# Kernel tuning notes

Measured on AMD Instinct MI355X. Metric: run time of the kernel, lower is better.

## Reference

```python
import jax, jax.numpy as jnp
import numpy as np

NB, NA, NC, NH, NW = 32, 5, 80, 76, 76
MAX_OBJ = 50
STRIDE = 32.0
ANCHORS_PX = np.array([18.3274, 21.6763, 59.9827, 66.0010, 106.8298,
                       175.1789, 252.2502, 112.8890, 312.6566, 293.3850], dtype=np.float32)
ANCHORS = (ANCHORS_PX / STRIDE).reshape(NA, 2)  # grid units, as in forward()
NOOBJ_SCALE, OBJ_SCALE = 1.0, 5.0
SIL_THRESH = 0.6
SEEN = 20000
COORD_SCALE, CLASS_SCALE = 1.0, 1.0
WARM = SEEN < 12800  # static python branch, matches `if seen < 12800`


def setup_inputs() -> dict:
    key = jax.random.key(0)
    k1, k2, k3, k4 = jax.random.split(key, 4)
    output = jax.random.normal(k1, (NB, NA * (5 + NC), NH, NW), dtype=jnp.float32) * 0.5
    # target layout per object: [class, cx, cy, w, h], coords normalized to (0,1)
    cls_id = jax.random.randint(k2, (NB, MAX_OBJ, 1), 0, NC).astype(jnp.float32)
    cxy = jax.random.uniform(k3, (NB, MAX_OBJ, 2), minval=0.05, maxval=0.95)
    wh = jax.random.uniform(k4, (NB, MAX_OBJ, 2), minval=0.02, maxval=0.4)
    target = jnp.concatenate([cls_id, cxy, wh], axis=-1).reshape(NB, MAX_OBJ * 5)
    return {"output": output, "target": target}


def _iou_cwh(a, b):
    # boxes as (cx, cy, w, h), broadcastable [..., 4]; darknet bbox_iou(x1y1x2y2=False)
    iw = jnp.maximum(jnp.minimum(a[..., 0] + a[..., 2] * 0.5, b[..., 0] + b[..., 2] * 0.5)
                     - jnp.maximum(a[..., 0] - a[..., 2] * 0.5, b[..., 0] - b[..., 2] * 0.5), 0.0)
    ih = jnp.maximum(jnp.minimum(a[..., 1] + a[..., 3] * 0.5, b[..., 1] + b[..., 3] * 0.5)
                     - jnp.maximum(a[..., 1] - a[..., 3] * 0.5, b[..., 1] - b[..., 3] * 0.5), 0.0)
    inter = iw * ih
    union = a[..., 2] * a[..., 3] + b[..., 2] * b[..., 3] - inter
    return inter / union


def reference(output, target):
    # ---- Part 1: parse raw predictions ----
    out = output.reshape(NB, NA, 5 + NC, NH, NW)
    x = jax.nn.sigmoid(out[:, :, 0])        # [B,A,H,W]
    y = jax.nn.sigmoid(out[:, :, 1])
    w = out[:, :, 2]
    h = out[:, :, 3]
    conf = jax.nn.sigmoid(out[:, :, 4])
    # cls layout matches view(nB*nA,nC,nH*nW).transpose(1,2) -> [B*A*H*W, C]
    cls_logits = jnp.transpose(out[:, :, 5:], (0, 1, 3, 4, 2)).reshape(-1, NC)

    # ---- Part 2: decode boxes (detached, like pred_boxes built from .data) ----
    anchors = jnp.asarray(ANCHORS)
    pbx = x + jnp.arange(NW, dtype=jnp.float32)[None, None, None, :]
    pby = y + jnp.arange(NH, dtype=jnp.float32)[None, None, :, None]
    pbw = jnp.exp(w) * anchors[None, :, 0, None, None]
    pbh = jnp.exp(h) * anchors[None, :, 1, None, None]
    pred_boxes = jax.lax.stop_gradient(jnp.stack([pbx, pby, pbw, pbh], axis=-1))  # [B,A,H,W,4]

    # ---- Part 3: build_targets, fully vectorized ----
    tgt = target.reshape(NB, MAX_OBJ, 5)
    valid = jnp.cumprod(tgt[:, :, 1] > 0, axis=1).astype(bool)  # break at first x==0
    gcls = tgt[:, :, 0]
    gx = tgt[:, :, 1] * NW
    gy = tgt[:, :, 2] * NH
    gw = tgt[:, :, 3] * NW
    gh = tgt[:, :, 4] * NH
    gt = jnp.stack([gx, gy, gw, gh], axis=-1)  # [B,T,4]

    # silence mask: max IoU of every pred box vs every gt box  -> [B,T,A,H,W]
    ious = _iou_cwh(pred_boxes[:, None], gt[:, :, None, None, None, :])
    max_iou = jnp.max(jnp.where(valid[:, :, None, None, None], ious, 0.0), axis=1)
    conf_mask = jnp.where(max_iou > SIL_THRESH, 0.0, NOOBJ_SCALE)  # [B,A,H,W]

    # best anchor per gt: IoU of centered (0,0,w,h) boxes -> closed form
    aw, ah = anchors[:, 0], anchors[:, 1]
    inter = jnp.minimum(gw[..., None], aw) * jnp.minimum(gh[..., None], ah)
    union = gw[..., None] * gh[..., None] + aw * ah - inter
    best_n = jnp.argmax(inter / union, axis=-1)  # [B,T]

    gi = gx.astype(jnp.int32)
    gj = gy.astype(jnp.int32)
    b_idx = jnp.arange(NB)[:, None]
    best_aw = anchors[best_n, 0]
    best_ah = anchors[best_n, 1]
    pred_at = pred_boxes[b_idx, best_n, gj, gi]  # [B,T,4]
    best_iou = _iou_cwh(gt, pred_at)             # [B,T]

    total = NB * NA * NH * NW
    flat = ((b_idx * NA + best_n) * NH + gj) * NW + gi
    flat = jnp.where(valid, flat, total).ravel()  # invalid objects -> dropped

    def scat(base, vals):
        return (jnp.full((total,), base, dtype=jnp.float32)
                .at[flat].set(vals.ravel(), mode='drop')
                .reshape(NB, NA, NH, NW))

    ones_t = jnp.ones_like(gx)
    warm = 1.0 if WARM else 0.0
    coord_mask = scat(warm, ones_t)
    cls_mask = scat(0.0, ones_t)
    tx = scat(0.5 * warm, gx - gi)
    ty = scat(0.5 * warm, gy - gj)
    tw = scat(0.0, jnp.log(gw / best_aw))
    th = scat(0.0, jnp.log(gh / best_ah))
    tconf = scat(0.0, best_iou)
    tcls = scat(0.0, gcls)
    conf_mask = (conf_mask.ravel()
                 .at[flat].set(jnp.full(flat.shape, OBJ_SCALE, dtype=jnp.float32), mode='drop')
                 .reshape(NB, NA, NH, NW))
    conf_mask = jnp.sqrt(conf_mask)

    # ---- Part 4: losses ----
    loss_x = COORD_SCALE * jnp.sum((x * coord_mask - tx * coord_mask) ** 2) / 2.0
    loss_y = COORD_SCALE * jnp.sum((y * coord_mask - ty * coord_mask) ** 2) / 2.0
    loss_w = COORD_SCALE * jnp.sum((w * coord_mask - tw * coord_mask) ** 2) / 2.0
    loss_h = COORD_SCALE * jnp.sum((h * coord_mask - th * coord_mask) ** 2) / 2.0
    loss_conf = jnp.sum((conf * conf_mask - tconf * conf_mask) ** 2) / 2.0
    logp = jax.nn.log_softmax(cls_logits, axis=-1)
    labels = tcls.ravel().astype(jnp.int32)
    nll = -jnp.take_along_axis(logp, labels[:, None], axis=1)[:, 0]
    loss_cls = CLASS_SCALE * jnp.sum(nll * cls_mask.ravel())

    return loss_x + loss_y + loss_w + loss_h + loss_conf + loss_cls
```

## Files before the change

### kernel.cpp

```cpp
#include <hip/hip_runtime.h>
#include <math.h>

#define NBATCH 32
#define NANCH  5
#define NCLS   80
#define NHH    76
#define NWW    76
#define MAXOBJ 50
#define CSZ    (NHH*NWW)
#define CELLS_PER_B (NANCH*CSZ)
#define NCH    (5+NCLS)
#define SILT   0.6f
#define CPT    4
#define BLK    256

__constant__ float c_aw[NANCH] = {18.3274f/32.0f, 59.9827f/32.0f, 106.8298f/32.0f, 252.2502f/32.0f, 312.6566f/32.0f};
__constant__ float c_ah[NANCH] = {21.6763f/32.0f, 66.0010f/32.0f, 175.1789f/32.0f, 112.8890f/32.0f, 293.3850f/32.0f};

__device__ __forceinline__ float sigf(float x) { return 1.0f / (1.0f + __expf(-x)); }

__global__ void obj_kernel(const float* __restrict__ out,
                           const float* __restrict__ tgt,
                           float* __restrict__ loss) {
    __shared__ float T[MAXOBJ*5];
    __shared__ int   key[MAXOBJ];
    const int b = blockIdx.x;
    const int t = threadIdx.x;
    for (int i = t; i < MAXOBJ*5; i += 64) T[i] = tgt[(size_t)b*MAXOBJ*5 + i];
    __syncthreads();

    float gx=0.f, gy=0.f, gw=0.f, gh=0.f;
    int gi=0, gj=0, bn=0, cls=0;
    bool valid = false;
    if (t < MAXOBJ) {
        valid = true;
        for (int j = 0; j <= t; ++j) valid = valid && (T[j*5+1] > 0.0f);
        cls = (int)T[t*5+0];
        gx = T[t*5+1]*NWW; gy = T[t*5+2]*NHH;
        gw = T[t*5+3]*NWW; gh = T[t*5+4]*NHH;
        gi = (int)gx; gj = (int)gy;
        float best = -1.0f;
        for (int a = 0; a < NANCH; ++a) {
            float inter = fminf(gw, c_aw[a]) * fminf(gh, c_ah[a]);
            float uni   = gw*gh + c_aw[a]*c_ah[a] - inter;
            float iou   = inter / uni;
            if (iou > best) { best = iou; bn = a; }
        }
        key[t] = valid ? (bn*CSZ + gj*NWW + gi) : (-1 - t);
    }
    __syncthreads();

    if (t < MAXOBJ && valid) {
        bool owner = true;
        for (int o2 = t+1; o2 < MAXOBJ; ++o2)
            if (key[o2] == key[t]) { owner = false; break; }
        if (owner) {
            const size_t base = ((size_t)(b*NANCH + bn))*NCH*CSZ + (size_t)(gj*NWW + gi);
            float xr = out[base];
            float yr = out[base + (size_t)CSZ];
            float wr = out[base + (size_t)2*CSZ];
            float hr = out[base + (size_t)3*CSZ];
            float cr = out[base + (size_t)4*CSZ];
            float sx = sigf(xr), sy = sigf(yr), sc = sigf(cr);
            float pw = __expf(wr)*c_aw[bn], ph = __expf(hr)*c_ah[bn];
            float px = sx + (float)gi, py = sy + (float)gj;
            float iw = fmaxf(fminf(px+pw*0.5f, gx+gw*0.5f) - fmaxf(px-pw*0.5f, gx-gw*0.5f), 0.0f);
            float ih = fmaxf(fminf(py+ph*0.5f, gy+gh*0.5f) - fmaxf(py-ph*0.5f, gy-gh*0.5f), 0.0f);
            float inter = iw*ih;
            float biou  = inter / (pw*ph + gw*gh - inter);
            float tx = gx - (float)gi, ty = gy - (float)gj;
            float tw = __logf(gw / c_aw[bn]), th = __logf(gh / c_ah[bn]);
            float l = 0.5f*((sx-tx)*(sx-tx) + (sy-ty)*(sy-ty)
                          + (wr-tw)*(wr-tw) + (hr-th)*(hr-th));
            l += 2.5f*(sc - biou)*(sc - biou);
            const float* lg = out + base + (size_t)5*CSZ;
            float m = -1e30f, s = 0.0f, lc = 0.0f;
            for (int c = 0; c < NCLS; ++c) {
                float L = lg[(size_t)c*CSZ];
                if (c == cls) lc = L;
                if (L > m) { s = s*__expf(m - L) + 1.0f; m = L; }
                else       { s += __expf(L - m); }
            }
            l += m + __logf(s) - lc;
            atomicAdd(loss, l);
        }
    }
}

__global__ __launch_bounds__(BLK)
void cell_kernel(const float* __restrict__ out,
                 const float* __restrict__ tgt,
                 float* __restrict__ loss) {
    __shared__ float  T[MAXOBJ*5];
    __shared__ float4 sbox[MAXOBJ];
    __shared__ float2 sak[MAXOBJ];
    __shared__ float  wsum[BLK/64];
    const int b = blockIdx.y;
    const int t = threadIdx.x;
    for (int i = t; i < MAXOBJ*5; i += BLK) T[i] = tgt[(size_t)b*MAXOBJ*5 + i];
    __syncthreads();
    if (t < MAXOBJ) {
        bool valid = true;
        for (int j = 0; j <= t; ++j) valid = valid && (T[j*5+1] > 0.0f);
        float gx = T[t*5+1]*NWW, gy = T[t*5+2]*NHH;
        float gw = T[t*5+3]*NWW, gh = T[t*5+4]*NHH;
        int bn = 0; float best = -1.0f;
        for (int a = 0; a < NANCH; ++a) {
            float inter = fminf(gw, c_aw[a]) * fminf(gh, c_ah[a]);
            float uni   = gw*gh + c_aw[a]*c_ah[a] - inter;
            float iou   = inter / uni;
            if (iou > best) { best = iou; bn = a; }
        }
        int k = valid ? (bn*CSZ + ((int)gy)*NWW + (int)gx) : (-1 - t);
        if (valid) {
            sbox[t] = make_float4(gx - gw*0.5f, gy - gh*0.5f, gx + gw*0.5f, gy + gh*0.5f);
            sak[t]  = make_float2(gw*gh, __int_as_float(k));
        } else {
            sbox[t] = make_float4(3e8f, 3e8f, 3e8f, 3e8f);
            sak[t]  = make_float2(1.0f, __int_as_float(k));
        }
    }
    __syncthreads();

    const int c0 = blockIdx.x*(BLK*CPT) + t;
    float px1[CPT], py1[CPT], px2[CPT], py2[CPT], pa[CPT], crs[CPT];
    int cc[CPT]; bool live[CPT];
    #pragma unroll
    for (int k = 0; k < CPT; ++k) {
        const int c = c0 + k*BLK;
        cc[k] = c;
        live[k] = (c < CELLS_PER_B);
        float xr=0.f, yr=0.f, wr=0.f, hr=0.f, cr=0.f;
        int a = 0;
        if (live[k]) {
            a = c / CSZ;
            const int rem = c - a*CSZ;
            const size_t base = ((size_t)(b*NANCH + a))*NCH*CSZ + (size_t)rem;
            xr = out[base];
            yr = out[base + (size_t)CSZ];
            wr = out[base + (size_t)2*CSZ];
            hr = out[base + (size_t)3*CSZ];
            cr = out[base + (size_t)4*CSZ];
        }
        const int rem = c - a*CSZ;
        const int i = rem % NWW;
        const int j = rem / NWW;
        float pw = __expf(wr)*c_aw[a], ph = __expf(hr)*c_ah[a];
        float px = sigf(xr) + (float)i, py = sigf(yr) + (float)j;
        px1[k] = px - pw*0.5f; px2[k] = px + pw*0.5f;
        py1[k] = py - ph*0.5f; py2[k] = py + ph*0.5f;
        pa[k]  = pw*ph; crs[k] = cr;
    }

    bool sil[CPT], own[CPT];
    #pragma unroll
    for (int k = 0; k < CPT; ++k) { sil[k] = false; own[k] = false; }

    for (int o = 0; o < MAXOBJ; ++o) {
        const float4 bb = sbox[o];
        const float2 ak = sak[o];
        const int bkey = __float_as_int(ak.y);
        #pragma unroll
        for (int k = 0; k < CPT; ++k) {
            float iw = fmaxf(fminf(px2[k], bb.z) - fmaxf(px1[k], bb.x), 0.0f);
            float ih = fmaxf(fminf(py2[k], bb.w) - fmaxf(py1[k], bb.y), 0.0f);
            float inter = iw*ih;
            sil[k] = sil[k] || (inter > SILT*(pa[k] + ak.x - inter));
            own[k] = own[k] || (bkey == cc[k]);
        }
    }

    float l = 0.0f;
    #pragma unroll
    for (int k = 0; k < CPT; ++k) {
        if (live[k] && !own[k] && !sil[k]) {
            float sc = sigf(crs[k]);
            l += 0.5f*sc*sc;
        }
    }
    for (int off = 32; off > 0; off >>= 1) l += __shfl_down(l, off);
    if ((t & 63) == 0) wsum[t >> 6] = l;
    __syncthreads();
    if (t == 0) {
        float s = 0.0f;
        for (int w = 0; w < BLK/64; ++w) s += wsum[w];
        atomicAdd(loss, s);
    }
}

extern "C" void kernel_launch(void* const* d_in, const int* in_sizes, int n_in,
                              void* d_out, int out_size, void* d_ws, size_t ws_size,
                              hipStream_t stream) {
    const float* out = (const float*)d_in[0];
    const float* tgt = (const float*)d_in[1];
    float* loss = (float*)d_out;
    hipMemsetAsync(loss, 0, (size_t)out_size*sizeof(float), stream);
    obj_kernel<<<NBATCH, 64, 0, stream>>>(out, tgt, loss);
    dim3 grid((CELLS_PER_B + BLK*CPT - 1)/(BLK*CPT), NBATCH);
    cell_kernel<<<grid, BLK, 0, stream>>>(out, tgt, loss);
}
```

Baseline: 445.1 us.

## Fuse object and cell kernels, vectorize loads, spread atomics across slots

Merges the per-object kernel into the cell kernel as extra blocks, one block per object. Inside those blocks the class softmax is computed across a wavefront with shuffles, where it was previously a serial loop. Cell threads now load 4 contiguous cells with float4, and the silence test is rewritten as a max-reduced linear threshold, which drops the per-cell owner-key comparison. The owner cell's noobj term is instead subtracted in the object path. Atomics go to 256 strided slots and are summed by a small reduce kernel, which cuts contention at the cost of an extra launch.

```diff
diff --git a/kernel.cpp b/kernel.cpp
--- a/kernel.cpp
+++ b/kernel.cpp
@@ -10,181 +10,208 @@
 #define CSZ    (NHH*NWW)
 #define CELLS_PER_B (NANCH*CSZ)
 #define NCH    (5+NCLS)
-#define SILT   0.6f
 #define CPT    4
 #define BLK    256
+#define TCG    (CELLS_PER_B/CPT)
+#define NCBLK  ((TCG + BLK - 1)/BLK)
+#define NSLOT  256
+#define SLOTSTRIDE 16
 
 __constant__ float c_aw[NANCH] = {18.3274f/32.0f, 59.9827f/32.0f, 106.8298f/32.0f, 252.2502f/32.0f, 312.6566f/32.0f};
 __constant__ float c_ah[NANCH] = {21.6763f/32.0f, 66.0010f/32.0f, 175.1789f/32.0f, 112.8890f/32.0f, 293.3850f/32.0f};
 
 __device__ __forceinline__ float sigf(float x) { return 1.0f / (1.0f + __expf(-x)); }
 
-__global__ void obj_kernel(const float* __restrict__ out,
-                           const float* __restrict__ tgt,
-                           float* __restrict__ loss) {
-    __shared__ float T[MAXOBJ*5];
-    __shared__ int   key[MAXOBJ];
-    const int b = blockIdx.x;
-    const int t = threadIdx.x;
-    for (int i = t; i < MAXOBJ*5; i += 64) T[i] = tgt[(size_t)b*MAXOBJ*5 + i];
-    __syncthreads();
-
-    float gx=0.f, gy=0.f, gw=0.f, gh=0.f;
-    int gi=0, gj=0, bn=0, cls=0;
-    bool valid = false;
-    if (t < MAXOBJ) {
-        valid = true;
-        for (int j = 0; j <= t; ++j) valid = valid && (T[j*5+1] > 0.0f);
-        cls = (int)T[t*5+0];
-        gx = T[t*5+1]*NWW; gy = T[t*5+2]*NHH;
-        gw = T[t*5+3]*NWW; gh = T[t*5+4]*NHH;
-        gi = (int)gx; gj = (int)gy;
-        float best = -1.0f;
-        for (int a = 0; a < NANCH; ++a) {
-            float inter = fminf(gw, c_aw[a]) * fminf(gh, c_ah[a]);
-            float uni   = gw*gh + c_aw[a]*c_ah[a] - inter;
-            float iou   = inter / uni;
-            if (iou > best) { best = iou; bn = a; }
-        }
-        key[t] = valid ? (bn*CSZ + gj*NWW + gi) : (-1 - t);
-    }
-    __syncthreads();
-
-    if (t < MAXOBJ && valid) {
-        bool owner = true;
-        for (int o2 = t+1; o2 < MAXOBJ; ++o2)
-            if (key[o2] == key[t]) { owner = false; break; }
-        if (owner) {
-            const size_t base = ((size_t)(b*NANCH + bn))*NCH*CSZ + (size_t)(gj*NWW + gi);
-            float xr = out[base];
-            float yr = out[base + (size_t)CSZ];
-            float wr = out[base + (size_t)2*CSZ];
-            float hr = out[base + (size_t)3*CSZ];
-            float cr = out[base + (size_t)4*CSZ];
-            float sx = sigf(xr), sy = sigf(yr), sc = sigf(cr);
-            float pw = __expf(wr)*c_aw[bn], ph = __expf(hr)*c_ah[bn];
-            float px = sx + (float)gi, py = sy + (float)gj;
-            float iw = fmaxf(fminf(px+pw*0.5f, gx+gw*0.5f) - fmaxf(px-pw*0.5f, gx-gw*0.5f), 0.0f);
-            float ih = fmaxf(fminf(py+ph*0.5f, gy+gh*0.5f) - fmaxf(py-ph*0.5f, gy-gh*0.5f), 0.0f);
-            float inter = iw*ih;
-            float biou  = inter / (pw*ph + gw*gh - inter);
-            float tx = gx - (float)gi, ty = gy - (float)gj;
-            float tw = __logf(gw / c_aw[bn]), th = __logf(gh / c_ah[bn]);
-            float l = 0.5f*((sx-tx)*(sx-tx) + (sy-ty)*(sy-ty)
-                          + (wr-tw)*(wr-tw) + (hr-th)*(hr-th));
-            l += 2.5f*(sc - biou)*(sc - biou);
-            const float* lg = out + base + (size_t)5*CSZ;
-            float m = -1e30f, s = 0.0f, lc = 0.0f;
-            for (int c = 0; c < NCLS; ++c) {
-                float L = lg[(size_t)c*CSZ];
-                if (c == cls) lc = L;
-                if (L > m) { s = s*__expf(m - L) + 1.0f; m = L; }
-                else       { s += __expf(L - m); }
-            }
-            l += m + __logf(s) - lc;
-            atomicAdd(loss, l);
-        }
-    }
-}
-
 __global__ __launch_bounds__(BLK)
-void cell_kernel(const float* __restrict__ out,
-                 const float* __restrict__ tgt,
-                 float* __restrict__ loss) {
+void region_kernel(const float* __restrict__ out,
+                   const float* __restrict__ tgt,
+                   float* __restrict__ acc) {
     __shared__ float  T[MAXOBJ*5];
     __shared__ float4 sbox[MAXOBJ];
-    __shared__ float2 sak[MAXOBJ];
+    __shared__ float  sthr[MAXOBJ];
+    __shared__ int    keyS[MAXOBJ];
+    __shared__ int    valS[MAXOBJ];
     __shared__ float  wsum[BLK/64];
     const int b = blockIdx.y;
     const int t = threadIdx.x;
     for (int i = t; i < MAXOBJ*5; i += BLK) T[i] = tgt[(size_t)b*MAXOBJ*5 + i];
     __syncthreads();
-    if (t < MAXOBJ) {
-        bool valid = true;
-        for (int j = 0; j <= t; ++j) valid = valid && (T[j*5+1] > 0.0f);
-        float gx = T[t*5+1]*NWW, gy = T[t*5+2]*NHH;
-        float gw = T[t*5+3]*NWW, gh = T[t*5+4]*NHH;
-        int bn = 0; float best = -1.0f;
-        for (int a = 0; a < NANCH; ++a) {
-            float inter = fminf(gw, c_aw[a]) * fminf(gh, c_ah[a]);
-            float uni   = gw*gh + c_aw[a]*c_ah[a] - inter;
-            float iou   = inter / uni;
-            if (iou > best) { best = iou; bn = a; }
-        }
-        int k = valid ? (bn*CSZ + ((int)gy)*NWW + (int)gx) : (-1 - t);
-        if (valid) {
-            sbox[t] = make_float4(gx - gw*0.5f, gy - gh*0.5f, gx + gw*0.5f, gy + gh*0.5f);
-            sak[t]  = make_float2(gw*gh, __int_as_float(k));
+
+    const int slot = ((blockIdx.y*gridDim.x + blockIdx.x) & (NSLOT-1)) * SLOTSTRIDE;
+
+    if (blockIdx.x < NCBLK) {
+        if (t < MAXOBJ) {
+            bool valid = true;
+            for (int j2 = 0; j2 <= t; ++j2) valid = valid && (T[j2*5+1] > 0.0f);
+            float gx = T[t*5+1]*NWW, gy = T[t*5+2]*NHH;
+            float gw = T[t*5+3]*NWW, gh = T[t*5+4]*NHH;
+            if (valid) {
+                sbox[t] = make_float4(gx - gw*0.5f, gy - gh*0.5f, gx + gw*0.5f, gy + gh*0.5f);
+                float area = gw*gh;
+                sthr[t] = 0.375f*area;
+            } else {
+                sbox[t] = make_float4(3e8f, 3e8f, 3e8f, 3e8f);
+                sthr[t] = 1.0f;
+            }
+        }
+        __syncthreads();
+
+        const int  tc   = blockIdx.x*BLK + t;
+        const bool live = tc < TCG;
+        const int  c    = tc*CPT;
+        const int  a    = c / CSZ;
+        const int  rem  = c - a*CSZ;
+        const int  jj   = rem / NWW;
+        const int  i0   = rem - jj*NWW;
+
+        float xr[CPT], yr[CPT], wr[CPT], hr[CPT], cf[CPT];
+        if (live) {
+            const float* base = out + ((size_t)(b*NANCH + a)*NCH)*CSZ + rem;
+            float4 v;
+            v = *(const float4*)(base);        xr[0]=v.x; xr[1]=v.y; xr[2]=v.z; xr[3]=v.w;
+            v = *(const float4*)(base+  CSZ);  yr[0]=v.x; yr[1]=v.y; yr[2]=v.z; yr[3]=v.w;
+            v = *(const float4*)(base+2*CSZ);  wr[0]=v.x; wr[1]=v.y; wr[2]=v.z; wr[3]=v.w;
+            v = *(const float4*)(base+3*CSZ);  hr[0]=v.x; hr[1]=v.y; hr[2]=v.z; hr[3]=v.w;
+            v = *(const float4*)(base+4*CSZ);  cf[0]=v.x; cf[1]=v.y; cf[2]=v.z; cf[3]=v.w;
         } else {
-            sbox[t] = make_float4(3e8f, 3e8f, 3e8f, 3e8f);
-            sak[t]  = make_float2(1.0f, __int_as_float(k));
-        }
-    }
-    __syncthreads();
-
-    const int c0 = blockIdx.x*(BLK*CPT) + t;
-    float px1[CPT], py1[CPT], px2[CPT], py2[CPT], pa[CPT], crs[CPT];
-    int cc[CPT]; bool live[CPT];
-    #pragma unroll
-    for (int k = 0; k < CPT; ++k) {
-        const int c = c0 + k*BLK;
-        cc[k] = c;
-        live[k] = (c < CELLS_PER_B);
-        float xr=0.f, yr=0.f, wr=0.f, hr=0.f, cr=0.f;
-        int a = 0;
-        if (live[k]) {
-            a = c / CSZ;
-            const int rem = c - a*CSZ;
-            const size_t base = ((size_t)(b*NANCH + a))*NCH*CSZ + (size_t)rem;
-            xr = out[base];
-            yr = out[base + (size_t)CSZ];
-            wr = out[base + (size_t)2*CSZ];
-            hr = out[base + (size_t)3*CSZ];
-            cr = out[base + (size_t)4*CSZ];
-        }
-        const int rem = c - a*CSZ;
-        const int i = rem % NWW;
-        const int j = rem / NWW;
-        float pw = __expf(wr)*c_aw[a], ph = __expf(hr)*c_ah[a];
-        float px = sigf(xr) + (float)i, py = sigf(yr) + (float)j;
-        px1[k] = px - pw*0.5f; px2[k] = px + pw*0.5f;
-        py1[k] = py - ph*0.5f; py2[k] = py + ph*0.5f;
-        pa[k]  = pw*ph; crs[k] = cr;
-    }
-
-    bool sil[CPT], own[CPT];
-    #pragma unroll
-    for (int k = 0; k < CPT; ++k) { sil[k] = false; own[k] = false; }
-
-    for (int o = 0; o < MAXOBJ; ++o) {
-        const float4 bb = sbox[o];
-        const float2 ak = sak[o];
-        const int bkey = __float_as_int(ak.y);
+            #pragma unroll
+            for (int k = 0; k < CPT; ++k) { xr[k]=yr[k]=wr[k]=hr[k]=cf[k]=0.0f; }
+        }
+
+        float px1[CPT], px2[CPT], py1[CPT], py2[CPT], qa[CPT], silv[CPT];
         #pragma unroll
         for (int k = 0; k < CPT; ++k) {
-            float iw = fmaxf(fminf(px2[k], bb.z) - fmaxf(px1[k], bb.x), 0.0f);
-            float ih = fmaxf(fminf(py2[k], bb.w) - fmaxf(py1[k], bb.y), 0.0f);
+            float pw = __expf(wr[k])*c_aw[a], ph = __expf(hr[k])*c_ah[a];
+            float px = sigf(xr[k]) + (float)(i0 + k);
+            float py = sigf(yr[k]) + (float)jj;
+            px1[k] = px - pw*0.5f; px2[k] = px + pw*0.5f;
+            py1[k] = py - ph*0.5f; py2[k] = py + ph*0.5f;
+            float pa = pw*ph;
+            qa[k]  = 0.375f*pa;
+            silv[k] = -1e30f;
+        }
+
+        for (int o = 0; o < MAXOBJ; ++o) {
+            const float4 bb  = sbox[o];
+            const float  thr = sthr[o];
+            #pragma unroll
+            for (int k = 0; k < CPT; ++k) {
+                float iw = fminf(px2[k], bb.z) - fmaxf(px1[k], bb.x);
+                float ih = fminf(py2[k], bb.w) - fmaxf(py1[k], bb.y);
+                iw = fmaxf(iw, 0.0f); ih = fmaxf(ih, 0.0f);
+                float inter = iw*ih;
+                silv[k] = fmaxf(silv[k], inter - (qa[k] + thr));
+            }
+        }
+
+        float l = 0.0f;
+        if (live) {
+            #pragma unroll
+            for (int k = 0; k < CPT; ++k) {
+                if (silv[k] <= 0.0f) {
+                    float sc = sigf(cf[k]);
+                    l += 0.5f*sc*sc;
+                }
+            }
+        }
+        for (int off = 32; off > 0; off >>= 1) l += __shfl_down(l, off);
+        if ((t & 63) == 0) wsum[t >> 6] = l;
+        __syncthreads();
+        if (t == 0) atomicAdd(acc + slot, wsum[0]+wsum[1]+wsum[2]+wsum[3]);
+
+    } else {
+        const int o = blockIdx.x - NCBLK;
+        if (t < MAXOBJ) {
+            bool valid = true;
+            for (int j2 = 0; j2 <= t; ++j2) valid = valid && (T[j2*5+1] > 0.0f);
+            valS[t] = valid ? 1 : 0;
+            if (valid) {
+                float gw = T[t*5+3]*NWW, gh = T[t*5+4]*NHH;
+                int bn = 0; float best = -1.0f;
+                for (int a = 0; a < NANCH; ++a) {
+                    float inter = fminf(gw, c_aw[a]) * fminf(gh, c_ah[a]);
+                    float uni   = gw*gh + c_aw[a]*c_ah[a] - inter;
+                    float iou   = inter / uni;
+                    if (iou > best) { best = iou; bn = a; }
+                }
+                int gi = (int)(T[t*5+1]*NWW), gj = (int)(T[t*5+2]*NHH);
+                keyS[t] = bn*CSZ + gj*NWW + gi;
+            } else keyS[t] = -1 - t;
+        }
+        __syncthreads();
+        if (t >= 64) return;
+        if (!valS[o]) return;
+        const int mykey = keyS[o];
+        bool owner = true;
+        for (int l2 = o+1; l2 < MAXOBJ; ++l2) owner = owner && (keyS[l2] != mykey);
+        if (!owner) return;
+
+        const float gx = T[o*5+1]*NWW, gy = T[o*5+2]*NHH;
+        const float gw = T[o*5+3]*NWW, gh = T[o*5+4]*NHH;
+        const int   cls = (int)T[o*5+0];
+        const int   bn  = mykey / CSZ;
+        const int   gi  = (int)gx, gj = (int)gy;
+        const float* base = out + ((size_t)(b*NANCH + bn)*NCH)*CSZ + (size_t)(gj*NWW + gi);
+        const float xr = base[0], yv = base[CSZ], wv = base[2*(size_t)CSZ];
+        const float hv = base[3*(size_t)CSZ], cv = base[4*(size_t)CSZ];
+        const float sx = sigf(xr), sy = sigf(yv), sc = sigf(cv);
+        const float pw = __expf(wv)*c_aw[bn], ph = __expf(hv)*c_ah[bn];
+        const float px = sx + (float)gi, py = sy + (float)gj;
+        const float pa = pw*ph;
+        const float qa = 0.375f*pa;
+
+        bool pred = false;
+        if (t < MAXOBJ && valS[t]) {
+            float ox = T[t*5+1]*NWW, oy = T[t*5+2]*NHH;
+            float ow = T[t*5+3]*NWW, oh = T[t*5+4]*NHH;
+            float iw = fminf(px + pw*0.5f, ox + ow*0.5f) - fmaxf(px - pw*0.5f, ox - ow*0.5f);
+            float ih = fminf(py + ph*0.5f, oy + oh*0.5f) - fmaxf(py - ph*0.5f, oy - oh*0.5f);
+            iw = fmaxf(iw, 0.0f); ih = fmaxf(ih, 0.0f);
             float inter = iw*ih;
-            sil[k] = sil[k] || (inter > SILT*(pa[k] + ak.x - inter));
-            own[k] = own[k] || (bkey == cc[k]);
+            float area = ow*oh;
+            float thr  = 0.375f*area;
+            pred = (inter - (qa + thr)) > 0.0f;
+        }
+        const bool silent = (__ballot(pred) != 0ull);
+
+        const float* lg = base + (size_t)5*CSZ;
+        const float L1 = lg[(size_t)t*CSZ];
+        const float L2 = (t < NCLS-64) ? lg[(size_t)(t+64)*CSZ] : -1e30f;
+        float m = fmaxf(L1, L2);
+        for (int off = 32; off > 0; off >>= 1) m = fmaxf(m, __shfl_xor(m, off));
+        float s = __expf(L1 - m) + ((t < NCLS-64) ? __expf(L2 - m) : 0.0f);
+        for (int off = 32; off > 0; off >>= 1) s += __shfl_xor(s, off);
+        const float lc = (cls < 64) ? __shfl(L1, cls) : __shfl(L2, cls - 64);
+
+        if (t == 0) {
+            float iw = fminf(px + pw*0.5f, gx + gw*0.5f) - fmaxf(px - pw*0.5f, gx - gw*0.5f);
+            float ih = fminf(py + ph*0.5f, gy + gh*0.5f) - fmaxf(py - ph*0.5f, gy - gh*0.5f);
+            iw = fmaxf(iw, 0.0f); ih = fmaxf(ih, 0.0f);
+            float inter = iw*ih;
+            float biou  = inter / (pa + gw*gh - inter);
+            float tx = gx - (float)gi, ty = gy - (float)gj;
+            float tw = __logf(gw / c_aw[bn]), th = __logf(gh / c_ah[bn]);
+            float l = 0.5f*((sx-tx)*(sx-tx) + (sy-ty)*(sy-ty)
+                          + (wv-tw)*(wv-tw) + (hv-th)*(hv-th));
+            l += 2.5f*(sc - biou)*(sc - biou);
+            l += m + __logf(s) - lc;
+            if (!silent) l -= 0.5f*sc*sc;
+            atomicAdd(acc + slot, l);
         }
     }
-
-    float l = 0.0f;
-    #pragma unroll
-    for (int k = 0; k < CPT; ++k) {
-        if (live[k] && !own[k] && !sil[k]) {
-            float sc = sigf(crs[k]);
-            l += 0.5f*sc*sc;
-        }
-    }
+}
+
+__global__ void reduce_kernel(const float* __restrict__ acc, float* __restrict__ loss) {
+    __shared__ float wsum[NSLOT/64];
+    const int t = threadIdx.x;
+    float l = acc[t*SLOTSTRIDE];
     for (int off = 32; off > 0; off >>= 1) l += __shfl_down(l, off);
     if ((t & 63) == 0) wsum[t >> 6] = l;
     __syncthreads();
     if (t == 0) {
         float s = 0.0f;
-        for (int w = 0; w < BLK/64; ++w) s += wsum[w];
-        atomicAdd(loss, s);
+        for (int w = 0; w < NSLOT/64; ++w) s += wsum[w];
+        loss[0] = s;
     }
 }
 
@@ -193,9 +220,10 @@
                               hipStream_t stream) {
     const float* out = (const float*)d_in[0];
     const float* tgt = (const float*)d_in[1];
+    float* acc  = (float*)d_ws;
     float* loss = (float*)d_out;
-    hipMemsetAsync(loss, 0, (size_t)out_size*sizeof(float), stream);
-    obj_kernel<<<NBATCH, 64, 0, stream>>>(out, tgt, loss);
-    dim3 grid((CELLS_PER_B + BLK*CPT - 1)/(BLK*CPT), NBATCH);
-    cell_kernel<<<grid, BLK, 0, stream>>>(out, tgt, loss);
+    hipMemsetAsync(acc, 0, (size_t)NSLOT*SLOTSTRIDE*sizeof(float), stream);
+    dim3 grid(NCBLK + MAXOBJ, NBATCH);
+    region_kernel<<<grid, BLK, 0, stream>>>(out, tgt, acc);
+    reduce_kernel<<<1, NSLOT, 0, stream>>>(acc, loss);
 }
```

Measured after the change: 376.9 us. 15.3% less time.
